# Optimization experiments

Measured on AMD Instinct MI355X. Metric: run time of the kernel, lower is better.

Reference implementation:

```python
import math
import jax, jax.numpy as jnp
import numpy as np
from jax import lax

jax.config.update("jax_enable_x64", True)

DECOMP_LEVEL = 5
# Daubechies-5 (db5) decomposition low-pass filter (pywt convention)
_DB5_LO = np.array([0.003335725285001549, -0.012580751999015526, -0.006241490213011705,
                    0.07757149384006515, -0.03224486958502952, -0.24229488706619015,
                    0.13842814590110342, 0.7243085284385744, 0.6038292697974729,
                    0.160102397974125], dtype=np.float64)
_L = _DB5_LO.size
_DB5_HI = _DB5_LO[::-1].copy() * ((-1.0) ** np.arange(_L))  # QMF high-pass
LO = jnp.asarray(_DB5_LO, jnp.float32)
HI = jnp.asarray(_DB5_HI, jnp.float32)
LOR = jnp.asarray(_DB5_LO[::-1].copy(), jnp.float32)
HIR = jnp.asarray(_DB5_HI[::-1].copy(), jnp.float32)


def _an_last(x):
    # orthonormal periodized analysis along last axis: (..., n) -> (..., n/2) x2
    n = x.shape[-1]
    lead = x.shape[:-1]
    xp = jnp.concatenate([x, x[..., : _L - 2]], axis=-1).reshape(-1, 1, n + _L - 2)
    k = jnp.stack([LO, HI])[:, None, :]  # (2,1,L)
    y = lax.conv_general_dilated(xp, k, (2,), "VALID")  # (B,2,n/2)
    y = y.reshape(lead + (2, n // 2))
    return y[..., 0, :], y[..., 1, :]


def _syn_last(a, d):
    # exact transpose/inverse of _an_last (orthonormal -> W^T = W^-1)
    n2 = a.shape[-1]
    n = 2 * n2
    lead = a.shape[:-1]
    B = int(np.prod(lead)) if lead else 1
    u = jnp.zeros((B, 2, n), a.dtype)
    u = u.at[:, 0, ::2].set(a.reshape(B, n2))
    u = u.at[:, 1, ::2].set(d.reshape(B, n2))
    up = jnp.concatenate([u[..., -(_L - 1):], u], axis=-1)  # circular left pad
    k = jnp.stack([LOR, HIR])[None, :, :]  # (1,2,L)
    y = lax.conv_general_dilated(up, k, (1,), "VALID")  # (B,1,n)
    return y.reshape(lead + (n,))


def _dwt2(x):  # x: (C,h,w) -> ll, lh, hl, hh each (C,h/2,w/2)
    a_h, d_h = _an_last(x.swapaxes(-1, -2))
    a_h = a_h.swapaxes(-1, -2)
    d_h = d_h.swapaxes(-1, -2)
    ll, lh = _an_last(a_h)
    hl, hh = _an_last(d_h)
    return ll, lh, hl, hh


def _idwt2(ll, lh, hl, hh):
    a_h = _syn_last(ll, lh)
    d_h = _syn_last(hl, hh)
    return _syn_last(a_h.swapaxes(-1, -2), d_h.swapaxes(-1, -2)).swapaxes(-1, -2)


def _estimate_noise(data):
    p = data.shape[0]
    rr = data @ data.T
    rri = jnp.linalg.inv(rr + 1e-6 * jnp.eye(p, dtype=data.dtype))
    def per_band(i):
        xx = rri - jnp.outer(rri[:, i], rri[i, :]) / rri[i, i]
        beta = xx @ rr[:, i]
        return beta.at[i].set(0.0)
    betas = jax.vmap(per_band)(jnp.arange(p))  # (p,p)
    return data - betas @ data


def hyres_forward(x):
    H, W, K = x.shape
    N = H * W
    data = x.reshape(N, K).T.astype(jnp.float64)
    w = _estimate_noise(data)
    omega1 = (jnp.sqrt(jnp.var(w, axis=1, ddof=1)) + 1e-30) ** 2  # (K,) f64
    y_w = x * omega1 ** -0.5  # whitened, f64
    u, s, v_pca = jnp.linalg.svd(y_w.reshape(N, K), full_matrices=False)
    pc = (u * s).reshape(W, H, K).astype(jnp.float32).transpose(2, 0, 1)  # (K,H,W)
    # multi-level 2D DWT per channel
    ll = pc
    highs = []
    for _ in range(DECOMP_LEVEL):
        ll, lh, hl, hh = _dwt2(ll)
        highs.append((lh, hl, hh))
    # overwrite-style full coefficient image [[LL,LH],[HL,HH]] recursively
    full = ll
    for lh, hl, hh in reversed(highs):
        top = jnp.concatenate([full, lh], axis=-1)
        bot = jnp.concatenate([hl, hh], axis=-1)
        full = jnp.concatenate([top, bot], axis=-2)
    V = full.transpose(1, 2, 0).reshape(N, K)
    V2 = V * V
    norm_v = jnp.sum(V2)
    n_xyz = jnp.asarray(V.size, jnp.float32)
    col_norm = jnp.sum(V2, axis=0)  # (K,)
    # SURE of soft-threshold over a 15-point grid in [0, sqrt(log N)]
    ts = np.linspace(0.0, math.sqrt(math.log(N)), 15).astype(np.float32)
    sure_cols = []
    for t in ts:
        t2 = float(t * t)
        s_t = (jnp.sum(jnp.minimum(V2, t2), axis=0)
               + 2.0 * jnp.sum((V2 > t2).astype(jnp.float32), axis=0)
               - col_norm)
        sure_cols.append(s_t)
    sure_all = jnp.stack(sure_cols, axis=1)  # (K,15)
    c_const = norm_v - n_xyz
    # replicate the in-place cumulative update: S_r = sum_{j<r} S_j + sure_r + C
    def step(acc, sure_r):
        s_r = acc + sure_r + c_const
        return acc + s_r, jnp.min(s_r)
    _, min_sure = lax.scan(step, jnp.zeros((15,), jnp.float32), sure_all)
    # early-exit: first rank>1 where min_sure increases; else loop ends at K-1
    cond = min_sure[2:] > min_sure[1:-1]
    rank = jnp.where(jnp.any(cond), 2 + jnp.argmax(cond), K - 1)
    mask = (jnp.arange(K) < rank).astype(jnp.float32)[:, None, None]
    # truncation-to-rank == zeroing channels >= rank (inverse DWT is linear)
    y = ll * mask
    for lh, hl, hh in reversed(highs):
        y = _idwt2(y, lh * mask, hl * mask, hh * mask)
    y_est = y.transpose(1, 2, 0).reshape(N, K)  # zero cols beyond rank
    out = (omega1.astype(jnp.float32) ** 0.5) * (y_est @ v_pca.astype(jnp.float32)).reshape(H, W, K)
    return out


def setup_inputs() -> dict:
    key = jax.random.key(0)
    k1, k2, k3 = jax.random.split(key, 3)
    H = W = 384
    K = 191
    R = 8  # low-rank spectral structure + noise, as HyRes assumes
    a = jax.random.normal(k1, (H * W, R), jnp.float32)
    b = jax.random.normal(k2, (R, K), jnp.float32)
    x = (a @ b) / np.sqrt(R) + 0.1 * jax.random.normal(k3, (H * W, K), jnp.float32)
    return {"x": x.reshape(H, W, K)}


def reference(x):
    return hyres_forward(x)
```

## Files before the change

### kernel.cpp

```cpp
#include <hip/hip_runtime.h>
#include <math.h>

#define K_     191
#define LD     192
#define N_     147456
#define MSUB   16
#define NT     15
#define TRI_N  18336
#define SMEM_CHOL  ((TRI_N + 1056 + 64) * 8)
#define SMEM_SOLVE ((TRI_N + 192 + 192 + 192) * 8)
#define SMEM2_SZ (6880 * 8 + 32 * 4 + TRI_N * 4)

#define NPAIR  6
#define NSPLIT 256
#define CHUNK  (N_ / NSPLIT)
#define RSTEP  16

__constant__ float c_lo[10] = {
  0.003335725285001549f, -0.012580751999015526f, -0.006241490213011705f,
  0.07757149384006515f,  -0.03224486958502952f, -0.24229488706619015f,
  0.13842814590110342f,   0.7243085284385744f,   0.6038292697974729f,
  0.160102397974125f };
__constant__ float c_hi[10] = {
  0.160102397974125f,    -0.6038292697974729f,   0.7243085284385744f,
 -0.13842814590110342f,  -0.24229488706619015f,  0.03224486958502952f,
  0.07757149384006515f,   0.006241490213011705f,-0.012580751999015526f,
 -0.003335725285001549f };

__global__ __launch_bounds__(256, 6) void k_rr(const float* __restrict__ x,
                                               double* __restrict__ rrg,
                                               double* __restrict__ m)
{
  __shared__ float Asf[2][RSTEP][64];
  __shared__ float Bsf[2][RSTEP][64];

  const int bid   = blockIdx.x;
  const int split = bid & (NSPLIT - 1);
  const int pair  = bid >> 8;
  const int BI[6] = {0, 0, 0, 1, 1, 2};
  const int BJ[6] = {0, 1, 2, 1, 2, 2};
  const int bi = BI[pair], bj = BJ[pair];
  const int diag = (bi == bj);
  const int ca = bi * 64, cb = bj * 64;

  const int t  = threadIdx.x;
  const int tx = t & 15, ty = t >> 4;
  const int mycol = t & 63, rowgrp = t >> 6;
  const long n0 = (long)split * CHUNK;

  double acc[4][4];
  #pragma unroll
  for (int v = 0; v < 4; ++v)
    #pragma unroll
    for (int u = 0; u < 4; ++u) acc[v][u] = 0.0;
  double csum = 0.0;

  float ra[4], rbv[4];
  const int cA = ca + mycol, cB = cb + mycol;
  const bool okA = (cA < K_), okB = (cB < K_);

  auto LOADT = [&](int r0) {
    #pragma unroll
    for (int i = 0; i < 4; ++i) {
      int row = i * 4 + rowgrp;
      long gr = (n0 + r0 + row) * (long)K_;
      float va = okA ? x[gr + cA] : 0.f;
      ra[i] = va;
      if (diag) csum += (double)va;
      else      rbv[i] = okB ? x[gr + cB] : 0.f;
    }
  };
  auto WRITET = [&](int buf) {
    #pragma unroll
    for (int i = 0; i < 4; ++i) {
      int row = i * 4 + rowgrp;
      Asf[buf][row][mycol] = ra[i];
      if (!diag) Bsf[buf][row][mycol] = rbv[i];
    }
  };

  LOADT(0);
  WRITET(0);
  __syncthreads();

  int cur = 0;
  for (int r0 = 0; r0 < CHUNK; r0 += RSTEP) {
    const bool hasnext = (r0 + RSTEP < CHUNK);
    if (hasnext) LOADT(r0 + RSTEP);
    const float (*As)[64] = Asf[cur];
    const float (*Bs)[64] = diag ? Asf[cur] : Bsf[cur];
    #pragma unroll 4
    for (int k = 0; k < RSTEP; ++k) {
      double a0 = (double)As[k][ty],      a1 = (double)As[k][ty + 16];
      double a2 = (double)As[k][ty + 32], a3 = (double)As[k][ty + 48];
      double b0 = (double)Bs[k][tx],      b1 = (double)Bs[k][tx + 16];
      double b2 = (double)Bs[k][tx + 32], b3 = (double)Bs[k][tx + 48];
      acc[0][0] += a0 * b0; acc[0][1] += a0 * b1; acc[0][2] += a0 * b2; acc[0][3] += a0 * b3;
      acc[1][0] += a1 * b0; acc[1][1] += a1 * b1; acc[1][2] += a1 * b2; acc[1][3] += a1 * b3;
      acc[2][0] += a2 * b0; acc[2][1] += a2 * b1; acc[2][2] += a2 * b2; acc[2][3] += a2 * b3;
      acc[3][0] += a3 * b0; acc[3][1] += a3 * b1; acc[3][2] += a3 * b2; acc[3][3] += a3 * b3;
    }
    if (hasnext) WRITET(cur ^ 1);
    __syncthreads();
    cur ^= 1;
  }

  #pragma unroll
  for (int v = 0; v < 4; ++v) {
    int mrow = ca + ty + 16 * v;
    #pragma unroll
    for (int u = 0; u < 4; ++u) {
      int ncol = cb + tx + 16 * u;
      if (mrow < K_ && ncol < K_ && (!diag || mrow <= ncol))
        atomicAdd(&rrg[(size_t)mrow * K_ + ncol], acc[v][u]);
    }
  }

  if (diag) {
    double* sc = (double*)Bsf;
    sc[t] = csum;
    __syncthreads();
    if (t < 64) {
      int c = ca + t;
      if (c < K_) {
        double s = sc[t] + sc[t + 64] + sc[t + 128] + sc[t + 192];
        atomicAdd(&m[c], s);
      }
    }
  }
}

__global__ __launch_bounds__(256) void k_reduce(const double* __restrict__ rrg,
                                                double* __restrict__ rr)
{
  int idx = blockIdx.x * 256 + threadIdx.x;
  if (idx >= TRI_N) return;
  int i = (int)((sqrtf(8.f * (float)idx + 1.f) - 1.f) * 0.5f);
  while ((i + 1) * (i + 2) / 2 <= idx) ++i;
  while (i * (i + 1) / 2 > idx) --i;
  int j = idx - (i * (i + 1)) / 2;
  double s = rrg[(size_t)j * K_ + i];
  rr[i * LD + j] = s;
  rr[j * LD + i] = s;
}

__global__ __launch_bounds__(512) void k_chol(
    const double* __restrict__ rr, double* __restrict__ Lg,
    double* __restrict__ rdg)
{
  extern __shared__ double smem[];
  double* tri  = smem;
  double* tmp  = smem + TRI_N;
  double* tmp2 = tmp + 1056;
  const int t = threadIdx.x;

  for (int i = t >> 5; i < K_; i += 16) {
    int base = (i * (i + 1)) / 2;
    for (int j = t & 31; j <= i; j += 32) {
      double v = rr[i * LD + j];
      tri[base + j] = (i == j) ? v + 1e-6 : v;
    }
  }
  __syncthreads();

  for (int J = 0; J < 6; ++J) {
    const int j0 = J * 32;
    const int nb = (K_ - j0 < 32) ? (K_ - j0) : 32;

    if (t < 64) {
      const int rl = t & 31;
      double a[32];
      #pragma unroll
      for (int c = 0; c < 32; ++c) {
        int i = j0 + rl;
        a[c] = (c <= rl && rl < nb) ? tri[(i * (i + 1)) / 2 + j0 + c] : 0.0;
      }
      #pragma unroll
      for (int k = 0; k < 32; ++k) {
        double akk = __shfl(a[k], k);
        double piv = sqrt(akk);
        double inv = 1.0 / piv;
        if (t == k) {
          tmp2[k] = inv;
          if (j0 + k < K_) rdg[j0 + k] = inv;
        }
        a[k] = (rl == k) ? piv : a[k] * inv;
        #pragma unroll
        for (int c = k + 1; c < 32; ++c) {
          double lck = __shfl(a[k], c);
          if (c <= rl) a[c] -= a[k] * lck;
        }
      }
      if (t < 32 && rl < nb) {
        int i = j0 + rl;
        int rb = (i * (i + 1)) / 2 + j0;
        #pragma unroll
        for (int c = 0; c < 32; ++c)
          if (c <= rl) tri[rb + c] = a[c];
      }
    }
    if (t < 32) {
      const int c = t;
      double xcol[32];
      #pragma unroll
      for (int r = 0; r < 32; ++r) {
        int rr_ = (j0 + r < K_) ? j0 + r : K_ - 1;
        int rb2 = (rr_ * (rr_ + 1)) / 2 + j0;
        double s = (r == c) ? 1.0 : 0.0;
        #pragma unroll
        for (int k = 0; k < 32; ++k)
          if (k < r) s -= tri[rb2 + k] * xcol[k];
        xcol[r] = s * tmp2[r];
      }
      #pragma unroll
      for (int r = 0; r < 32; ++r)
        tmp[r * 33 + c] = (r >= c) ? xcol[r] : 0.0;
    }
    __syncthreads();

    {
      int p = j0 + 32 + t;
      if (nb == 32 && p < K_) {
        int pb = (p * (p + 1)) / 2 + j0;
        double arow[32];
        #pragma unroll
        for (int k = 0; k < 32; ++k) arow[k] = tri[pb + k];
        #pragma unroll
        for (int c = 0; c < 32; ++c) {
          double s = 0.0;
          #pragma unroll
          for (int k = 0; k < 32; ++k)
            if (k <= c) s += arow[k] * tmp[c * 33 + k];
          tri[pb + c] = s;
        }
      }
    }
    __syncthreads();

    {
      int s0 = j0 + 32;
      int n = K_ - s0;
      if (n > 0) {
        int R4 = (n + 3) >> 2;
        int T4 = R4 * (R4 + 1) / 2;
        for (int tile = t; tile < T4; tile += 512) {
          int ti = (int)((sqrtf(8.f * (float)tile + 1.f) - 1.f) * 0.5f);
          while ((ti + 1) * (ti + 2) / 2 <= tile) ++ti;
          while (ti * (ti + 1) / 2 > tile) --ti;
          int tj = tile - ti * (ti + 1) / 2;
          int r0 = s0 + ti * 4, c0 = s0 + tj * 4;
          int rb[4], cb[4];
          #pragma unroll
          for (int u = 0; u < 4; ++u) {
            int r = (r0 + u < K_) ? r0 + u : K_ - 1;
            rb[u] = (r * (r + 1)) / 2;
            int c = (c0 + u < K_) ? c0 + u : K_ - 1;
            cb[u] = (c * (c + 1)) / 2;
          }
          double acc[4][4];
          #pragma unroll
          for (int u = 0; u < 4; ++u)
            #pragma unroll
            for (int v2 = 0; v2 < 4; ++v2) acc[u][v2] = 0.0;
          #pragma unroll 4
          for (int p = 0; p < 32; ++p) {
            double lr[4], lc[4];
            #pragma unroll
            for (int u = 0; u < 4; ++u) {
              lr[u] = tri[rb[u] + j0 + p];
              lc[u] = tri[cb[u] + j0 + p];
            }
            #pragma unroll
            for (int u = 0; u < 4; ++u)
              #pragma unroll
              for (int v2 = 0; v2 < 4; ++v2) acc[u][v2] += lr[u] * lc[v2];
          }
          #pragma unroll
          for (int u = 0; u < 4; ++u) {
            int r = r0 + u;
            if (r < K_) {
              #pragma unroll
              for (int v2 = 0; v2 < 4; ++v2) {
                int c = c0 + v2;
                if (c <= r) tri[rb[u] + c] -= acc[u][v2];
              }
            }
          }
        }
      }
    }
    __syncthreads();
  }

  for (int idx = t; idx < TRI_N; idx += 512) Lg[idx] = tri[idx];
}

__global__ __launch_bounds__(256) void k_csolve(
    const double* __restrict__ Lg, const double* __restrict__ rdg,
    const double* __restrict__ mg, double* __restrict__ s2g,
    double* __restrict__ zg)
{
  extern __shared__ double ssm[];
  double* Ls   = ssm;
  double* rd_s = Ls + TRI_N;
  double* m_sh = rd_s + 192;
  double* ys   = m_sh + 192;
  const int t = threadIdx.x;
  const int bid = blockIdx.x;

  const int start = (bid < K_) ? (bid * (bid + 1)) / 2 : 0;
  for (int idx = start + t; idx < TRI_N; idx += 256) Ls[idx] = Lg[idx];
  if (t < K_) { rd_s[t] = rdg[t]; m_sh[t] = mg[t]; }
  __syncthreads();

  if (t >= 64) return;
  const int l = t;

  if (bid < K_) {
    const int i = bid;
    double x0 = 0.0, x1 = 0.0, x2 = 0.0;
    {
      double rdi = rd_s[i];
      if ((i & 63) == l) {
        int sl = i >> 6;
        if (sl == 0) x0 = rdi; else if (sl == 1) x1 = rdi; else x2 = rdi;
      }
    }
    for (int r = i + 1; r < K_; ++r) {
      int rb = (r * (r + 1)) >> 1;
      double partial = 0.0;
      { int k = l;       if (k < r) partial += Ls[rb + k] * x0; }
      { int k = l + 64;  if (k < r) partial += Ls[rb + k] * x1; }
      { int k = l + 128; if (k < r) partial += Ls[rb + k] * x2; }
      #pragma unroll
      for (int mm = 32; mm > 0; mm >>= 1) partial += __shfl_xor(partial, mm);
      double val = -partial * rd_s[r];
      if ((r & 63) == l) {
        int sl = r >> 6;
        if (sl == 0) x0 = val; else if (sl == 1) x1 = val; else x2 = val;
      }
    }
    double s2p = x0 * x0 + x1 * x1 + x2 * x2;
    #pragma unroll
    for (int mm = 32; mm > 0; mm >>= 1) s2p += __shfl_xor(s2p, mm);
    if (l == 0) s2g[i] = s2p;
  } else {
    double y0 = 0.0, y1 = 0.0, y2 = 0.0;
    for (int r = 0; r < K_; ++r) {
      int rb = (r * (r + 1)) >> 1;
      double partial = 0.0;
      { int k = l;       if (k < r) partial += Ls[rb + k] * y0; }
      { int k = l + 64;  if (k < r) partial += Ls[rb + k] * y1; }
      { int k = l + 128; if (k < r) partial += Ls[rb + k] * y2; }
      #pragma unroll
      for (int mm = 32; mm > 0; mm >>= 1) partial += __shfl_xor(partial, mm);
      double val = (m_sh[r] - partial) * rd_s[r];
      if ((r & 63) == l) {
        int sl = r >> 6;
        if (sl == 0) y0 = val; else if (sl == 1) y1 = val; else y2 = val;
      }
      if (l == 0) ys[r] = val;
    }
    double z0 = 0.0, z1 = 0.0, z2 = 0.0;
    for (int r = K_ - 1; r >= 0; --r) {
      double partial = 0.0;
      { int k = l;       if (k > r && k < K_) partial += Ls[((k * (k + 1)) >> 1) + r] * z0; }
      { int k = l + 64;  if (k > r && k < K_) partial += Ls[((k * (k + 1)) >> 1) + r] * z1; }
      { int k = l + 128; if (k > r && k < K_) partial += Ls[((k * (k + 1)) >> 1) + r] * z2; }
      #pragma unroll
      for (int mm = 32; mm > 0; mm >>= 1) partial += __shfl_xor(partial, mm);
      double val = (ys[r] - partial) * rd_s[r];
      if ((r & 63) == l) {
        int sl = r >> 6;
        if (sl == 0) z0 = val; else if (sl == 1) z1 = val; else z2 = val;
      }
      if (l == 0) zg[r] = val;
    }
  }
}

__global__ __launch_bounds__(256) void k_finals(
    const double* __restrict__ rr, const double* __restrict__ s2g,
    const double* __restrict__ zg, double* __restrict__ invsq,
    float* __restrict__ normv)
{
  __shared__ double tmps[K_];
  const int t = threadIdx.x;
  if (t < K_) {
    double dii = s2g[t];
    double q = 1.0 / dii;
    double sm_ = zg[t] / dii;
    double var = (q - sm_ * sm_ / (double)N_) / (double)(N_ - 1);
    double t1 = sqrt(var) + 1e-30;
    double om = t1 * t1;
    invsq[t] = 1.0 / sqrt(om);
    tmps[t] = rr[t * LD + t] / om;
  }
  __syncthreads();
  if (t < 64) {
    double s = 0.0;
    for (int i = t; i < K_; i += 64) s += tmps[i];
    #pragma unroll
    for (int off = 32; off > 0; off >>= 1) s += __shfl_down(s, off);
    if (t == 0) *normv = (float)s;
  }
}

__device__ __forceinline__ void cholqr(double* shQ, double* shS, int t)
{
  if (t < MSUB * MSUB) {
    int a = t & (MSUB - 1), b = t >> 4;
    double s = 0.0;
    for (int r = 0; r < K_; ++r) s += shQ[r * MSUB + a] * shQ[r * MSUB + b];
    shS[b * 17 + a] = s;
  }
  __syncthreads();
  for (int k = 0; k < MSUB; ++k) {
    if (t == 0) shS[k * 17 + k] = sqrt(shS[k * 17 + k]);
    __syncthreads();
    if (t > k && t < MSUB) shS[t * 17 + k] /= shS[k * 17 + k];
    __syncthreads();
    if (t < MSUB * MSUB) {
      int r = t & (MSUB - 1), c = t >> 4;
      if (c > k && r >= c) shS[r * 17 + c] -= shS[r * 17 + k] * shS[c * 17 + k];
    }
    __syncthreads();
  }
  if (t < K_) {
    double q[MSUB];
    #pragma unroll
    for (int c = 0; c < MSUB; ++c) {
      double v = shQ[t * MSUB + c];
      for (int p = 0; p < c; ++p) v -= q[p] * shS[c * 17 + p];
      q[c] = v / shS[c * 17 + c];
    }
    #pragma unroll
    for (int c = 0; c < MSUB; ++c) shQ[t * MSUB + c] = q[c];
  }
  __syncthreads();
}

__global__ __launch_bounds__(512) void k_sub(
    const double* __restrict__ rr, const double* __restrict__ invsq,
    float* __restrict__ W1, float* __restrict__ W2)
{
  extern __shared__ double dsm[];
  double* shQ  = dsm;
  double* shZ  = shQ + 3056;
  double* shS  = shZ + 3056;
  double* Ws   = shS + 272;
  double* inv_s= Ws + 272;
  double* ev   = inv_s + 192;
  double* cs_  = ev + 16;
  double* sn_  = cs_ + 8;
  int* ipp  = (int*)(sn_ + 8);
  int* iqq  = ipp + 8;
  int* perm = iqq + 8;
  float* tri = (float*)(perm + 16);
  const int t = threadIdx.x;

  if (t < K_) inv_s[t] = invsq[t];
  __syncthreads();
  for (int i = t >> 4; i < K_; i += 32) {
    int base = (i * (i + 1)) / 2;
    double di = inv_s[i];
    for (int j = t & 15; j <= i; j += 16)
      tri[base + j] = (float)(rr[i * LD + j] * di * inv_s[j]);
  }
  __syncthreads();

  for (int idx = t; idx < K_ * MSUB; idx += 512) {
    int i = idx >> 4, c = idx & 15;
    float g = (i >= c) ? tri[(i * (i + 1)) / 2 + c] : tri[(c * (c + 1)) / 2 + i];
    shQ[idx] = (double)g;
  }
  __syncthreads();

  cholqr(shQ, shS, t);
  for (int it = 0; it < 4; ++it) {
    for (int idx = t; idx < K_ * MSUB; idx += 512) shZ[idx] = shQ[idx];
    __syncthreads();
    if (t < 96 * 4) {
      int i2 = t >> 2, c4 = t & 3;
      int r0 = 2 * i2, r1 = r0 + 1;
      int has1 = (r1 < K_);
      int rb0 = (r0 * (r0 + 1)) >> 1;
      int rb1 = has1 ? ((r1 * (r1 + 1)) >> 1) : rb0;
      int cb0 = c4 * 4;
      double s0a = 0.0, s0b = 0.0, s0c = 0.0, s0d = 0.0;
      double s1a = 0.0, s1b = 0.0, s1c = 0.0, s1d = 0.0;
      #pragma unroll 2
      for (int k = 0; k <= r0; ++k) {
        double g0 = (double)tri[rb0 + k];
        double g1 = (double)tri[rb1 + k];
        double za = shZ[k * MSUB + cb0],     zb = shZ[k * MSUB + cb0 + 1];
        double zc = shZ[k * MSUB + cb0 + 2], zd = shZ[k * MSUB + cb0 + 3];
        s0a += g0 * za; s0b += g0 * zb; s0c += g0 * zc; s0d += g0 * zd;
        s1a += g1 * za; s1b += g1 * zb; s1c += g1 * zc; s1d += g1 * zd;
      }
      if (has1) {
        double g0 = (double)tri[rb1 + r0];
        double g1 = (double)tri[rb1 + r1];
        double za = shZ[r1 * MSUB + cb0],     zb = shZ[r1 * MSUB + cb0 + 1];
        double zc = shZ[r1 * MSUB + cb0 + 2], zd = shZ[r1 * MSUB + cb0 + 3];
        s0a += g0 * za; s0b += g0 * zb; s0c += g0 * zc; s0d += g0 * zd;
        s1a += g1 * za; s1b += g1 * zb; s1c += g1 * zc; s1d += g1 * zd;
      }
      int kk = ((r1 + 1) * (r1 + 2)) >> 1;
      #pragma unroll 2
      for (int k = r1 + 1; k < K_; ++k) {
        double g0 = (double)tri[kk + r0];
        double g1 = (double)tri[kk + r1];
        double za = shZ[k * MSUB + cb0],     zb = shZ[k * MSUB + cb0 + 1];
        double zc = shZ[k * MSUB + cb0 + 2], zd = shZ[k * MSUB + cb0 + 3];
        s0a += g0 * za; s0b += g0 * zb; s0c += g0 * zc; s0d += g0 * zd;
        s1a += g1 * za; s1b += g1 * zb; s1c += g1 * zc; s1d += g1 * zd;
        kk += k + 1;
      }
      shQ[r0 * MSUB + cb0]     = s0a;
      shQ[r0 * MSUB + cb0 + 1] = s0b;
      shQ[r0 * MSUB + cb0 + 2] = s0c;
      shQ[r0 * MSUB + cb0 + 3] = s0d;
      if (has1) {
        shQ[r1 * MSUB + cb0]     = s1a;
        shQ[r1 * MSUB + cb0 + 1] = s1b;
        shQ[r1 * MSUB + cb0 + 2] = s1c;
        shQ[r1 * MSUB + cb0 + 3] = s1d;
      }
    }
    __syncthreads();
    if (it < 3) cholqr(shQ, shS, t);
  }
  if (t < MSUB * MSUB) {
    int a = t & 15, b = t >> 4;
    double s = 0.0;
    for (int r = 0; r < K_; ++r) s += shZ[r * MSUB + b] * shQ[r * MSUB + a];
    shS[b * 17 + a] = s;
  }
  if (t < MSUB * 17) Ws[t] = 0.0;
  __syncthreads();
  if (t < MSUB) Ws[t * 17 + t] = 1.0;
  __syncthreads();
  for (int sweep = 0; sweep < 6; ++sweep) {
    for (int round = 0; round < 15; ++round) {
      if (t < 8) {
        int ia = (t == 0) ? 0 : (1 + ((t - 1 + round) % 15));
        int ib = 1 + ((14 - t + round) % 15);
        int p = ia < ib ? ia : ib;
        int q = ia < ib ? ib : ia;
        double app = shS[p * 17 + p], aqq = shS[q * 17 + q], apq = shS[p * 17 + q];
        double c = 1.0, s = 0.0;
        if (fabs(apq) > 1e-30 * (fabs(app) + fabs(aqq)) && apq != 0.0) {
          double tau = (aqq - app) / (2.0 * apq);
          double tt = (tau >= 0.0 ? 1.0 : -1.0) / (fabs(tau) + sqrt(1.0 + tau * tau));
          c = 1.0 / sqrt(1.0 + tt * tt); s = tt * c;
        }
        cs_[t] = c; sn_[t] = s; ipp[t] = p; iqq[t] = q;
      }
      __syncthreads();
      if (t < 128) {
        int i = t & 15, mI = t >> 4;
        int p = ipp[mI], q = iqq[mI];
        double c = cs_[mI], s = sn_[mI];
        double u = shS[i * 17 + p], v = shS[i * 17 + q];
        shS[i * 17 + p] = c * u - s * v; shS[i * 17 + q] = s * u + c * v;
        double wu = Ws[i * 17 + p], wv = Ws[i * 17 + q];
        Ws[i * 17 + p] = c * wu - s * wv; Ws[i * 17 + q] = s * wu + c * wv;
      }
      __syncthreads();
      if (t < 128) {
        int j = t & 15, mI = t >> 4;
        int p = ipp[mI], q = iqq[mI];
        double c = cs_[mI], s = sn_[mI];
        double u = shS[p * 17 + j], v = shS[q * 17 + j];
        shS[p * 17 + j] = c * u - s * v; shS[q * 17 + j] = s * u + c * v;
      }
      __syncthreads();
    }
  }
  if (t == 0) {
    for (int i = 0; i < MSUB; ++i) { ev[i] = shS[i * 17 + i]; perm[i] = i; }
    for (int i = 0; i < MSUB; ++i) {
      int best = i;
      for (int j = i + 1; j < MSUB; ++j)
        if (ev[perm[j]] > ev[perm[best]]) best = j;
      int tp = perm[i]; perm[i] = perm[best]; perm[best] = tp;
    }
  }
  __syncthreads();
  for (int idx = t; idx < K_ * MSUB; idx += 512) {
    int i = idx >> 4, c = idx & 15;
    int pc_ = perm[c];
    double e = 0.0;
    #pragma unroll
    for (int p = 0; p < MSUB; ++p) e += shZ[i * MSUB + p] * Ws[p * 17 + pc_];
    W1[i * MSUB + c] = (float)(inv_s[i] * e);
    W2[c * K_ + i]   = (float)(e / inv_s[i]);
  }
}

__global__ __launch_bounds__(256) void k_pc(const float* __restrict__ x,
                                            const float* __restrict__ W1,
                                            float* __restrict__ pc)
{
  __shared__ float xs[32][192];
  __shared__ float w1s[K_ * MSUB];
  int t = threadIdx.x;
  long n0 = (long)blockIdx.x * 32;
  for (int idx = t; idx < K_ * MSUB; idx += 256) w1s[idx] = W1[idx];
  for (int idx = t; idx < 32 * K_; idx += 256) {
    int row = idx / K_, col = idx - row * K_;
    xs[row][col] = x[(n0 + row) * K_ + col];
  }
  __syncthreads();
  int c = t & 15, nl = t >> 4;
  float a0 = 0.f, a1 = 0.f;
  for (int k = 0; k < K_; ++k) {
    float w = w1s[k * MSUB + c];
    a0 += xs[nl][k] * w;
    a1 += xs[nl + 16][k] * w;
  }
  __syncthreads();
  float* ts = &xs[0][0];
  ts[c * 33 + nl]      = a0;
  ts[c * 33 + nl + 16] = a1;
  __syncthreads();
  for (int idx = t; idx < MSUB * 32; idx += 256) {
    int cc = idx >> 5, nn = idx & 31;
    pc[(size_t)cc * N_ + n0 + nn] = ts[cc * 33 + nn];
  }
}

__global__ __launch_bounds__(256) void k_dwtv(const float* __restrict__ in,
                                              float* __restrict__ outv, int s)
{
  long gid = (long)blockIdx.x * 256 + threadIdx.x;
  int h = s >> 1;
  long per = (long)h * s;
  if (gid >= MSUB * per) return;
  int ch = (int)(gid / per);
  long rem = gid - (long)ch * per;
  int r = (int)(rem / s);
  int col = (int)(rem - (long)r * s);
  const float* cin = in + (long)ch * s * s;
  float la = 0.f, ld_ = 0.f;
  int base = 2 * r;
  #pragma unroll
  for (int l = 0; l < 10; ++l) {
    int rr_ = base + l; if (rr_ >= s) rr_ -= s;
    float v = cin[(long)rr_ * s + col];
    la += c_lo[l] * v; ld_ += c_hi[l] * v;
  }
  float* cout = outv + (long)ch * s * s;
  cout[(long)r * s + col] = la;
  cout[(long)(h + r) * s + col] = ld_;
}

__global__ __launch_bounds__(256) void k_dwth(const float* __restrict__ inv,
                                              float* __restrict__ llout,
                                              float* __restrict__ coef,
                                              int s, long offL, int last)
{
  long gid = (long)blockIdx.x * 256 + threadIdx.x;
  int h = s >> 1;
  long per = (long)s * h;
  if (gid >= MSUB * per) return;
  int ch = (int)(gid / per);
  long rem = gid - (long)ch * per;
  int r = (int)(rem / h);
  int mcol = (int)(rem - (long)r * h);
  const float* row = inv + (long)ch * s * s + (long)r * s;
  float lo = 0.f, hi = 0.f;
  int base = 2 * mcol;
  #pragma unroll
  for (int l = 0; l < 10; ++l) {
    int cc = base + l; if (cc >= s) cc -= s;
    float v = row[cc];
    lo += c_lo[l] * v; hi += c_hi[l] * v;
  }
  float* cslab = coef + (size_t)ch * N_ + offL;
  if (r < h) {
    llout[(size_t)ch * h * h + (long)r * h + mcol] = lo;
    if (last) coef[(size_t)ch * N_ + 147312 + (long)r * h + mcol] = lo;
    cslab[(long)r * h + mcol] = hi;
  } else {
    int rd = r - h;
    cslab[(long)h * h + (long)rd * h + mcol] = lo;
    cslab[(long)2 * h * h + (long)rd * h + mcol] = hi;
  }
}

__global__ __launch_bounds__(256) void k_stats(const float* __restrict__ coef,
                                               float* __restrict__ stats)
{
  int ch = blockIdx.x;
  int t = threadIdx.x;
  float T2[NT];
  {
    double stop = sqrt(log(147456.0));
    double step = stop / 14.0;
    for (int i = 0; i < NT; ++i) {
      double td = (i == 14) ? stop : (double)i * step;
      float tf = (float)td;
      T2[i] = tf * tf;
    }
  }
  float cn = 0.f, sm[NT], ct[NT];
  #pragma unroll
  for (int i = 0; i < NT; ++i) { sm[i] = 0.f; ct[i] = 0.f; }
  const float* base = coef + (size_t)ch * N_;
  for (int idx = t; idx < N_; idx += 256) {
    float v = base[idx];
    float v2 = v * v;
    cn += v2;
    #pragma unroll
    for (int i = 0; i < NT; ++i) {
      sm[i] += fminf(v2, T2[i]);
      ct[i] += (v2 > T2[i]) ? 1.0f : 0.0f;
    }
  }
  __shared__ float red2[4][32];
  int lane = t & 63, wv = t >> 6;
  for (int a = 0; a < 31; ++a) {
    float val = (a == 0) ? cn : ((a < 16) ? sm[a - 1] : ct[a - 16]);
    #pragma unroll
    for (int off = 32; off > 0; off >>= 1) val += __shfl_down(val, off);
    if (lane == 0) red2[wv][a] = val;
  }
  __syncthreads();
  if (t < 31)
    stats[ch * 31 + t] = red2[0][t] + red2[1][t] + red2[2][t] + red2[3][t];
}

__global__ void k_rank(const float* __restrict__ stats,
                       const float* __restrict__ normv, int* __restrict__ rankp)
{
  if (threadIdx.x != 0 || blockIdx.x != 0) return;
  float c_const = *normv - 28164096.0f;
  float acc[NT];
  for (int i = 0; i < NT; ++i) acc[i] = 0.f;
  float minsure[MSUB];
  for (int r = 0; r < MSUB; ++r) {
    float cn = stats[r * 31 + 0];
    float mn = 3.4e38f;
    for (int i = 0; i < NT; ++i) {
      float sure = stats[r * 31 + 1 + i] + 2.0f * stats[r * 31 + 16 + i] - cn;
      float s_r = acc[i] + sure + c_const;
      acc[i] = acc[i] + s_r;
      if (s_r < mn) mn = s_r;
    }
    minsure[r] = mn;
  }
  int rank = -1;
  for (int r = 2; r < MSUB; ++r) {
    if (minsure[r] > minsure[r - 1]) { rank = r; break; }
  }
  if (rank < 0) rank = MSUB - 1;
  *rankp = rank;
}

__global__ __launch_bounds__(256) void k_out(const float* __restrict__ pc,
                                             const float* __restrict__ W2,
                                             const int* __restrict__ rankp,
                                             float* __restrict__ out)
{
  long gid = (long)blockIdx.x * 256 + threadIdx.x;
  int n = (int)(gid / K_);
  int j = (int)(gid - (long)n * K_);
  int rank = *rankp;
  float acc = 0.f;
  for (int c = 0; c < rank; ++c)
    acc += pc[(size_t)c * N_ + n] * W2[c * K_ + j];
  out[gid] = acc;
}

extern "C" void kernel_launch(void* const* d_in, const int* in_sizes, int n_in,
                              void* d_out, int out_size, void* d_ws, size_t ws_size,
                              hipStream_t stream)
{
  if (n_in < 1 || in_sizes[0] != N_ * K_) return;
  const float* x = (const float*)d_in[0];
  float* out = (float*)d_out;
  (void)out_size;

  char* w = (char*)d_ws;
  size_t off = 0;
  auto alloc = [&](size_t bytes) -> char* {
    char* p = w + off;
    off = (off + bytes + 255) & ~(size_t)255;
    return p;
  };
  double* m_    = (double*)alloc(K_ * 8);
  double* rrp   = (double*)alloc((size_t)K_ * K_ * 8);
  double* rr    = (double*)alloc((size_t)K_ * LD * 8);
  double* Lg    = (double*)alloc((size_t)TRI_N * 8);
  double* rdg   = (double*)alloc(192 * 8);
  double* s2g   = (double*)alloc(192 * 8);
  double* zg    = (double*)alloc(192 * 8);
  double* invsq = (double*)alloc(K_ * 8);
  float*  normv = (float*)alloc(256);
  float*  W1    = (float*)alloc((size_t)K_ * MSUB * 4);
  float*  W2    = (float*)alloc((size_t)MSUB * K_ * 4);
  float*  pc    = (float*)alloc((size_t)MSUB * N_ * 4);
  float*  tmpv  = (float*)alloc((size_t)MSUB * N_ * 4);
  float*  coef  = (float*)alloc((size_t)MSUB * N_ * 4);
  float*  curA  = (float*)alloc((size_t)MSUB * 192 * 192 * 4);
  float*  curB  = (float*)alloc((size_t)MSUB * 96 * 96 * 4);
  float*  stats = (float*)alloc((size_t)MSUB * 31 * 4);
  int*    rankp = (int*)alloc(256);
  if (off > ws_size) return;

  hipMemsetAsync(m_, 0, K_ * sizeof(double), stream);
  hipMemsetAsync(rrp, 0, (size_t)K_ * K_ * sizeof(double), stream);

  hipFuncSetAttribute(reinterpret_cast<const void*>(k_chol),
                      hipFuncAttributeMaxDynamicSharedMemorySize, SMEM_CHOL);
  hipFuncSetAttribute(reinterpret_cast<const void*>(k_csolve),
                      hipFuncAttributeMaxDynamicSharedMemorySize, SMEM_SOLVE);
  hipFuncSetAttribute(reinterpret_cast<const void*>(k_sub),
                      hipFuncAttributeMaxDynamicSharedMemorySize, SMEM2_SZ);

  k_rr<<<NPAIR * NSPLIT, 256, 0, stream>>>(x, rrp, m_);
  k_reduce<<<(TRI_N + 255) / 256, 256, 0, stream>>>(rrp, rr);
  k_chol<<<1, 512, SMEM_CHOL, stream>>>(rr, Lg, rdg);
  k_csolve<<<K_ + 1, 256, SMEM_SOLVE, stream>>>(Lg, rdg, m_, s2g, zg);
  k_finals<<<1, 256, 0, stream>>>(rr, s2g, zg, invsq, normv);
  k_sub<<<1, 512, SMEM2_SZ, stream>>>(rr, invsq, W1, W2);
  k_pc<<<N_ / 32, 256, 0, stream>>>(x, W1, pc);

  int   sizes[5] = {384, 192, 96, 48, 24};
  long  offs[5]  = {0, 110592, 138240, 145152, 146880};
  float* lls[5]  = {curA, curB, curA, curB, curA};
  const float* curin = pc;
  for (int lev = 0; lev < 5; ++lev) {
    int s = sizes[lev], h = s >> 1;
    long nth = (long)MSUB * h * s;
    k_dwtv<<<(int)((nth + 255) / 256), 256, 0, stream>>>(curin, tmpv, s);
    k_dwth<<<(int)((nth + 255) / 256), 256, 0, stream>>>(tmpv, lls[lev], coef,
                                                         s, offs[lev],
                                                         lev == 4 ? 1 : 0);
    curin = lls[lev];
  }

  k_stats<<<MSUB, 256, 0, stream>>>(coef, stats);
  k_rank<<<1, 64, 0, stream>>>(stats, normv, rankp);
  k_out<<<(N_ * K_) / 256, 256, 0, stream>>>(pc, W2, rankp, out);
}
```

Before: 1.475 ms.

## Fuse vertical and horizontal DWT passes into one tiled shared-memory kernel

Replaces the separate vertical and horizontal wavelet kernels with one kernel per level. Each block loads a 40x40 input tile with periodic wrap into LDS, does the vertical filter, then the horizontal filter, and writes the LL/LH/HL/HH outputs directly. This removes the intermediate tmpv buffer round trip through global memory and halves the DWT kernel launches, at the cost of halo redundancy and more blocks with modest per-block work. The DWT is a small part of the total pipeline, which is likely dominated by the covariance and output kernels.

```diff
diff --git a/kernel.cpp b/kernel.cpp
--- a/kernel.cpp
+++ b/kernel.cpp
@@ -631,62 +631,63 @@
   }
 }
 
-__global__ __launch_bounds__(256) void k_dwtv(const float* __restrict__ in,
-                                              float* __restrict__ outv, int s)
-{
-  long gid = (long)blockIdx.x * 256 + threadIdx.x;
-  int h = s >> 1;
-  long per = (long)h * s;
-  if (gid >= MSUB * per) return;
-  int ch = (int)(gid / per);
-  long rem = gid - (long)ch * per;
-  int r = (int)(rem / s);
-  int col = (int)(rem - (long)r * s);
-  const float* cin = in + (long)ch * s * s;
-  float la = 0.f, ld_ = 0.f;
-  int base = 2 * r;
-  #pragma unroll
-  for (int l = 0; l < 10; ++l) {
-    int rr_ = base + l; if (rr_ >= s) rr_ -= s;
-    float v = cin[(long)rr_ * s + col];
-    la += c_lo[l] * v; ld_ += c_hi[l] * v;
-  }
-  float* cout = outv + (long)ch * s * s;
-  cout[(long)r * s + col] = la;
-  cout[(long)(h + r) * s + col] = ld_;
-}
-
-__global__ __launch_bounds__(256) void k_dwth(const float* __restrict__ inv,
+__global__ __launch_bounds__(256) void k_dwt2(const float* __restrict__ in,
                                               float* __restrict__ llout,
                                               float* __restrict__ coef,
-                                              int s, long offL, int last)
-{
-  long gid = (long)blockIdx.x * 256 + threadIdx.x;
-  int h = s >> 1;
-  long per = (long)s * h;
-  if (gid >= MSUB * per) return;
-  int ch = (int)(gid / per);
-  long rem = gid - (long)ch * per;
-  int r = (int)(rem / h);
-  int mcol = (int)(rem - (long)r * h);
-  const float* row = inv + (long)ch * s * s + (long)r * s;
-  float lo = 0.f, hi = 0.f;
-  int base = 2 * mcol;
-  #pragma unroll
-  for (int l = 0; l < 10; ++l) {
-    int cc = base + l; if (cc >= s) cc -= s;
-    float v = row[cc];
-    lo += c_lo[l] * v; hi += c_hi[l] * v;
-  }
-  float* cslab = coef + (size_t)ch * N_ + offL;
-  if (r < h) {
-    llout[(size_t)ch * h * h + (long)r * h + mcol] = lo;
-    if (last) coef[(size_t)ch * N_ + 147312 + (long)r * h + mcol] = lo;
-    cslab[(long)r * h + mcol] = hi;
-  } else {
-    int rd = r - h;
-    cslab[(long)h * h + (long)rd * h + mcol] = lo;
-    cslab[(long)2 * h * h + (long)rd * h + mcol] = hi;
+                                              int s, long offL, int last,
+                                              int ntr)
+{
+  __shared__ float xin[40][41];
+  __shared__ float las[16][41];
+  __shared__ float lds_[16][41];
+  const int h = s >> 1;
+  const int t = threadIdx.x;
+  int bid = blockIdx.x;
+  int ch = bid / (ntr * ntr);
+  int rem = bid - ch * (ntr * ntr);
+  int tr = rem / ntr, tc = rem - tr * ntr;
+  int rv0 = tr * 16, mc0 = tc * 16;
+  const float* cin = in + (long)ch * s * s;
+
+  for (int idx = t; idx < 40 * 40; idx += 256) {
+    int i = idx / 40, c = idx - i * 40;
+    int gr = (2 * rv0 + i) % s;
+    int gc = (2 * mc0 + c) % s;
+    xin[i][c] = cin[(long)gr * s + gc];
+  }
+  __syncthreads();
+
+  for (int idx = t; idx < 16 * 40; idx += 256) {
+    int i = idx / 40, c = idx - i * 40;
+    float la = 0.f, ld = 0.f;
+    #pragma unroll
+    for (int l = 0; l < 10; ++l) {
+      float v = xin[2 * i + l][c];
+      la += c_lo[l] * v; ld += c_hi[l] * v;
+    }
+    las[i][c] = la; lds_[i][c] = ld;
+  }
+  __syncthreads();
+
+  {
+    int i = t >> 4, j = t & 15;
+    int rv = rv0 + i, mc = mc0 + j;
+    if (rv < h && mc < h) {
+      float ll = 0.f, lh = 0.f, hl = 0.f, hh = 0.f;
+      #pragma unroll
+      for (int l = 0; l < 10; ++l) {
+        float a = las[i][2 * j + l];
+        float d = lds_[i][2 * j + l];
+        ll += c_lo[l] * a; lh += c_hi[l] * a;
+        hl += c_lo[l] * d; hh += c_hi[l] * d;
+      }
+      float* cslab = coef + (size_t)ch * N_ + offL;
+      llout[(size_t)ch * h * h + (long)rv * h + mc] = ll;
+      if (last) coef[(size_t)ch * N_ + 147312 + (long)rv * h + mc] = ll;
+      cslab[(long)rv * h + mc] = lh;
+      cslab[(long)h * h + (long)rv * h + mc] = hl;
+      cslab[(long)2 * h * h + (long)rv * h + mc] = hh;
+    }
   }
 }
 
@@ -802,7 +803,6 @@
   float*  W1    = (float*)alloc((size_t)K_ * MSUB * 4);
   float*  W2    = (float*)alloc((size_t)MSUB * K_ * 4);
   float*  pc    = (float*)alloc((size_t)MSUB * N_ * 4);
-  float*  tmpv  = (float*)alloc((size_t)MSUB * N_ * 4);
   float*  coef  = (float*)alloc((size_t)MSUB * N_ * 4);
   float*  curA  = (float*)alloc((size_t)MSUB * 192 * 192 * 4);
   float*  curB  = (float*)alloc((size_t)MSUB * 96 * 96 * 4);
@@ -834,11 +834,10 @@
   const float* curin = pc;
   for (int lev = 0; lev < 5; ++lev) {
     int s = sizes[lev], h = s >> 1;
-    long nth = (long)MSUB * h * s;
-    k_dwtv<<<(int)((nth + 255) / 256), 256, 0, stream>>>(curin, tmpv, s);
-    k_dwth<<<(int)((nth + 255) / 256), 256, 0, stream>>>(tmpv, lls[lev], coef,
-                                                         s, offs[lev],
-                                                         lev == 4 ? 1 : 0);
+    int ntr = (h + 15) / 16;
+    k_dwt2<<<16 * ntr * ntr, 256, 0, stream>>>(curin, lls[lev], coef,
+                                               s, offs[lev],
+                                               lev == 4 ? 1 : 0, ntr);
     curin = lls[lev];
   }
 
```

Measured after the change: 1.462 ms. Within noise of the previous version (-0.9%).
